# Kernel optimization log

Hardware: AMD Instinct MI355X
Metric: run time of the kernel (lower is better)

The kernel has to match this reference:

```python
import jax, jax.numpy as jnp
import numpy as np

H, I, B, S = 3200, 12800, 8, 1024  # InternViT-6B MLP dims


def setup_inputs() -> dict:
    key = jax.random.key(0)
    ks = jax.random.split(key, 8)
    # int8-valued activations/weights stored as int32 (harness dtype set)
    hidden_states = jax.random.randint(ks[0], (B, S, H), -127, 128, dtype=jnp.int32)
    scale = jax.random.uniform(ks[1], (B * S,), dtype=jnp.float32) * 1e-3 + 1e-5
    w1 = jax.random.randint(ks[2], (I, H), -127, 128, dtype=jnp.int32)
    w1_scale = jax.random.uniform(ks[3], (I,), dtype=jnp.float32) * 1e-3 + 1e-5
    b1 = jax.random.normal(ks[4], (I,), dtype=jnp.float32) * 0.02
    w2 = jax.random.randint(ks[5], (H, I), -127, 128, dtype=jnp.int32)
    w2_scale = jax.random.uniform(ks[6], (H,), dtype=jnp.float32) * 1e-3 + 1e-5
    b2 = jax.random.normal(ks[7], (H,), dtype=jnp.float32) * 0.02
    return {"hidden_states": hidden_states, "scale": scale, "w1": w1,
            "w1_scale": w1_scale, "b1": b1, "w2": w2, "w2_scale": w2_scale, "b2": b2}


def _w8a8_linear(x_q, x_scale, w_q, w_scale, b):
    # enough that fp32 matmul reproduces the exact integer accumulator to
    # within float32 rounding of the final sum.
    acc = jnp.matmul(x_q.astype(jnp.float32), w_q.astype(jnp.float32).T)  # [T, out]
    out = acc * x_scale[:, None] * w_scale[None, :] + b[None, :]
    return out.astype(jnp.float16)


def reference(hidden_states, scale, w1, w1_scale, b1, w2, w2_scale, b2):
    bsz, seq, hidden = hidden_states.shape
    x_q = hidden_states.reshape(-1, hidden)                 # [T, H] int8 values
    # fc1: W8A8 -> fp16 with dynamic per-token input scale
    fc1_out = _w8a8_linear(x_q, scale, w1, w1_scale, b1)    # [T, I] fp16
    # fused gelu_and_quant: exact GELU, then per-token dynamic int8 re-quant
    g = jax.nn.gelu(fc1_out.astype(jnp.float32), approximate=False)  # [T, I]
    new_scale = jnp.max(jnp.abs(g), axis=-1) / 127.0        # dynamic per-token scale
    act_q = jnp.clip(jnp.round(g / new_scale[:, None]), -127, 127)  # int8 values
    # fc2: W8A8 -> fp16
    out = _w8a8_linear(act_q, new_scale, w2, w2_scale, b2)  # [T, H] fp16
    return out
```

## Files before the change

kernel.cpp:

```cpp
#include <hip/hip_runtime.h>
#include <hip/hip_bf16.h>
#include <hip/hip_fp16.h>

#define T_DIM 8192
#define H_DIM 3200
#define I_DIM 12800

typedef int v4i __attribute__((ext_vector_type(4)));
typedef int v16i __attribute__((ext_vector_type(16)));
typedef _Float16 h8 __attribute__((ext_vector_type(8)));

__device__ __forceinline__ void gload16(const void* g, void* l) {
    __builtin_amdgcn_global_load_lds(
        (const __attribute__((address_space(1))) unsigned int*)g,
        (__attribute__((address_space(3))) unsigned int*)l, 16, 0, 0);
}

__global__ __launch_bounds__(256) void repack_kernel(const int* __restrict__ src,
                                                     unsigned int* __restrict__ dst,
                                                     long n4) {
    long i = (long)blockIdx.x * blockDim.x + threadIdx.x;
    long stride = (long)gridDim.x * blockDim.x;
    for (; i < n4; i += stride) {
        int4 v = ((const int4*)src)[i];
        dst[i] = (unsigned int)((v.x & 255) | ((v.y & 255) << 8) |
                                ((v.z & 255) << 16) | ((v.w & 255) << 24));
    }
}

template <int EPI>
__global__ __launch_bounds__(512, 2) void gemm_i8_32x32(
    const signed char* __restrict__ A, long strideA,
    const signed char* __restrict__ B, long strideB,
    int Ntrue, int K, int ldc,
    const float* __restrict__ rowscale, const float* __restrict__ colscale,
    const float* __restrict__ bias, void* __restrict__ Cout) {
    __shared__ signed char lds[131072];
    signed char* ldsA = lds;
    signed char* ldsB = lds + 65536;

    const int tid = threadIdx.x;
    const int lane = tid & 63, wid = tid >> 6;
    const int wr = wid >> 2, wc = wid & 3;
    const int bm = blockIdx.x, bn = blockIdx.y;
    const long Arow0 = (long)bm * 256;
    const long Bcol0 = (long)bn * 256;

    int g_row[2], g_cg[2];
#pragma unroll
    for (int u = 0; u < 2; ++u) {
        const int ch = tid + (u << 9);
        const int block = ch >> 7;
        const int p = ch & 127;
        const int half = (p >> 6) & 1;
        const int p6 = p & 63;
        const int r15 = p6 >> 2;
        const int col = p6 & 3;
        const int q = col ^ ((r15 >> 1) & 3);
        g_row[u] = block * 32 + ((q & 1) << 4) + r15;
        g_cg[u] = (half << 1) | (q >> 1);
    }
    const signed char* Ag0 = A + (Arow0 + g_row[0]) * strideA + g_cg[0] * 16;
    const signed char* Ag1 = A + (Arow0 + g_row[1]) * strideA + g_cg[1] * 16;
    const signed char* Bg0 = B + (Bcol0 + g_row[0]) * strideB + g_cg[0] * 16;
    const signed char* Bg1 = B + (Bcol0 + g_row[1]) * strideB + g_cg[1] * 16;
    const int d0 = tid * 16, d1 = (tid + 512) * 16;

    const int NH = K >> 6;

#define STAGE_A(h)                                  \
    {                                               \
        const int hc_ = (h) < NH ? (h) : NH - 1;    \
        const long ko_ = (long)hc_ << 6;            \
        signed char* d_ = ldsA + (((h) & 3) << 14); \
        gload16(Ag0 + ko_, d_ + d0);                \
        gload16(Ag1 + ko_, d_ + d1);                \
    }
#define STAGE_B(h)                                  \
    {                                               \
        const int hc_ = (h) < NH ? (h) : NH - 1;    \
        const long ko_ = (long)hc_ << 6;            \
        signed char* d_ = ldsB + (((h) & 3) << 14); \
        gload16(Bg0 + ko_, d_ + d0);                \
        gload16(Bg1 + ko_, d_ + d1);                \
    }

    const int rl = lane & 31, qh = lane >> 5;
    const int r15 = rl & 15, qb = rl >> 4;
    const int colr = ((qh << 1) | qb) ^ ((r15 >> 1) & 3);
    const int roff = r15 * 64 + colr * 16;
    const int aoff = (wr * 4) * 2048 + roff;
    const int boff = (wc * 2) * 2048 + roff;

    v16i acc[4][2] = {};

    STAGE_A(0); STAGE_B(0); STAGE_A(1); STAGE_B(1); STAGE_A(2); STAGE_B(2);
    asm volatile("s_waitcnt vmcnt(8)");
    __builtin_amdgcn_s_barrier();

    for (int h = 0; h < NH; ++h) {
        const signed char* sA = ldsA + ((h & 3) << 14);
        const signed char* sB = ldsB + ((h & 3) << 14);
        v4i a0[4], a1[4], b0[2], b1[2];
#pragma unroll
        for (int m = 0; m < 4; ++m) {
            a0[m] = *(const v4i*)(sA + aoff + m * 2048);
            a1[m] = *(const v4i*)(sA + aoff + m * 2048 + 1024);
        }
#pragma unroll
        for (int n = 0; n < 2; ++n) {
            b0[n] = *(const v4i*)(sB + boff + n * 2048);
            b1[n] = *(const v4i*)(sB + boff + n * 2048 + 1024);
        }
        STAGE_A(h + 3);
        STAGE_B(h + 3);
        __builtin_amdgcn_s_setprio(1);
#pragma unroll
        for (int m = 0; m < 4; ++m)
#pragma unroll
            for (int n = 0; n < 2; ++n)
                acc[m][n] = __builtin_amdgcn_mfma_i32_32x32x32_i8(
                    a0[m], b0[n], acc[m][n], 0, 0, 0);
#pragma unroll
        for (int m = 0; m < 4; ++m)
#pragma unroll
            for (int n = 0; n < 2; ++n)
                acc[m][n] = __builtin_amdgcn_mfma_i32_32x32x32_i8(
                    a1[m], b1[n], acc[m][n], 0, 0, 0);
        __builtin_amdgcn_s_setprio(0);
        asm volatile("s_waitcnt vmcnt(8)");
        __builtin_amdgcn_s_barrier();
    }

    const int row0 = bm * 256 + wr * 128;
    const int col0 = bn * 256 + wc * 64;
    const int rbase = 4 * qh;
#pragma unroll
    for (int m = 0; m < 4; ++m) {
#pragma unroll
        for (int n = 0; n < 2; ++n) {
            const int col = col0 + n * 32 + rl;
            if (col < Ntrue) {
                const float cs = colscale[col];
                const float bs = bias[col];
#pragma unroll
                for (int g = 0; g < 4; ++g) {
#pragma unroll
                    for (int rr = 0; rr < 4; ++rr) {
                        const int row = row0 + m * 32 + rbase + 8 * g + rr;
                        float v = (float)acc[m][n][g * 4 + rr];
                        v = __fmul_rn(v, rowscale[row]);
                        v = __fmul_rn(v, cs);
                        v = __fadd_rn(v, bs);
                        _Float16 hh = (_Float16)v;
                        const size_t idx = (size_t)row * ldc + col;
                        if (EPI == 0) ((_Float16*)Cout)[idx] = hh;
                        else ((float*)Cout)[idx] = (float)hh;
                    }
                }
            }
        }
    }
#undef STAGE_A
#undef STAGE_B
}

__global__ __launch_bounds__(256) void gelu_quant(_Float16* __restrict__ fc1,
                                                  float* __restrict__ nscale) {
    __shared__ float gbuf[I_DIM];
    __shared__ float wmax[4];
    const int tid = threadIdx.x, lane = tid & 63, wid = tid >> 6;
    const long t = blockIdx.x;
    const h8* row = (const h8*)(fc1 + t * I_DIM);
    float lmax = 0.f;
    for (int c = tid; c < I_DIM / 8; c += 256) {
        h8 v = row[c];
#pragma unroll
        for (int j = 0; j < 8; ++j) {
            float x = (float)v[j];
            float e = erff(__fdiv_rn(x, 1.41421356237309504880f));
            float g = __fmul_rn(__fmul_rn(0.5f, x), __fadd_rn(1.0f, e));
            gbuf[c * 8 + j] = g;
            lmax = fmaxf(lmax, fabsf(g));
        }
    }
#pragma unroll
    for (int off = 32; off; off >>= 1) lmax = fmaxf(lmax, __shfl_xor(lmax, off, 64));
    if (lane == 0) wmax[wid] = lmax;
    __syncthreads();
    const float gmax = fmaxf(fmaxf(wmax[0], wmax[1]), fmaxf(wmax[2], wmax[3]));
    const float ns = gmax / 127.0f;
    if (tid == 0) nscale[t] = ns;
    unsigned long long* out = (unsigned long long*)(fc1 + t * I_DIM);
    for (int c = tid; c < I_DIM / 8; c += 256) {
        unsigned long long pk = 0;
#pragma unroll
        for (int j = 0; j < 8; ++j) {
            float qv = rintf(__fdiv_rn(gbuf[c * 8 + j], ns));
            qv = fminf(fmaxf(qv, -127.f), 127.f);
            pk |= ((unsigned long long)(unsigned char)(signed char)(int)qv) << (8 * j);
        }
        out[c] = pk;
    }
}

extern "C" void kernel_launch(void* const* d_in, const int* in_sizes, int n_in,
                              void* d_out, int out_size, void* d_ws, size_t ws_size,
                              hipStream_t stream) {
    const int* hs = (const int*)d_in[0];
    const float* scale = (const float*)d_in[1];
    const int* w1 = (const int*)d_in[2];
    const float* w1s = (const float*)d_in[3];
    const float* b1 = (const float*)d_in[4];
    const int* w2 = (const int*)d_in[5];
    const float* w2s = (const float*)d_in[6];
    const float* b2 = (const float*)d_in[7];

    char* ws = (char*)d_ws;
    signed char* xq = (signed char*)ws;
    signed char* w1q = xq + (size_t)T_DIM * H_DIM;
    signed char* w2q = w1q + (size_t)I_DIM * H_DIM;
    _Float16* fc1h = (_Float16*)(w2q + (size_t)H_DIM * I_DIM);
    const size_t fixed = (size_t)T_DIM * H_DIM + 2 * (size_t)I_DIM * H_DIM;

    int nc = 1;
    while (nc < 16) {
        size_t need = fixed + ((size_t)T_DIM / nc) * I_DIM * 2 +
                      ((size_t)T_DIM / nc) * 4 + 256;
        if (need <= ws_size) break;
        nc <<= 1;
    }
    const int chunkT = T_DIM / nc;
    float* nscale = (float*)((char*)fc1h + (size_t)chunkT * I_DIM * 2);

    repack_kernel<<<2048, 256, 0, stream>>>(hs, (unsigned int*)xq, (long)T_DIM * H_DIM / 4);
    repack_kernel<<<2048, 256, 0, stream>>>(w1, (unsigned int*)w1q, (long)I_DIM * H_DIM / 4);
    repack_kernel<<<2048, 256, 0, stream>>>(w2, (unsigned int*)w2q, (long)H_DIM * I_DIM / 4);

    const int n2tiles = (H_DIM + 255) / 256;
    for (int c = 0; c < nc; ++c) {
        const int t0 = c * chunkT;
        gemm_i8_32x32<0><<<dim3(chunkT / 256, I_DIM / 256), 512, 0, stream>>>(
            xq + (size_t)t0 * H_DIM, (long)H_DIM, w1q, (long)H_DIM,
            I_DIM, H_DIM, I_DIM,
            scale + t0, w1s, b1, (void*)fc1h);
        gelu_quant<<<chunkT, 256, 0, stream>>>(fc1h, nscale);
        gemm_i8_32x32<1><<<dim3(chunkT / 256, n2tiles), 512, 0, stream>>>(
            (const signed char*)fc1h, (long)I_DIM * 2, w2q, (long)I_DIM,
            H_DIM, I_DIM, H_DIM,
            nscale, w2s, b2,
            (void*)((float*)d_out + (size_t)t0 * H_DIM));
    }
}
```

Before: 1.055 ms.

## Shrink int8 GEMM tiles to 128x128 with 256 threads and 3-stage LDS ring

Replaces the 256x256, 512-thread int8 MFMA GEMM with a 128x128 tile on 256 threads (four waves, each still 64x64). The LDS pipeline drops from four buffers to a three-slot rotating ring with a single combined A+B staging macro. LDS use falls from 128KB to 48KB and launch bounds target three blocks per CU. The goal is higher occupancy and a larger grid, and the fc2 N dimension (3200) now divides exactly by 128. In exchange, each tile does less data reuse per byte loaded, so global and L2 traffic goes up, and the prefetch distance is shorter.

```diff
diff --git a/kernel.cpp b/kernel.cpp
--- a/kernel.cpp
+++ b/kernel.cpp
@@ -29,27 +29,27 @@
 }
 
 template <int EPI>
-__global__ __launch_bounds__(512, 2) void gemm_i8_32x32(
+__global__ __launch_bounds__(256, 3) void gemm_i8_128(
     const signed char* __restrict__ A, long strideA,
     const signed char* __restrict__ B, long strideB,
     int Ntrue, int K, int ldc,
     const float* __restrict__ rowscale, const float* __restrict__ colscale,
     const float* __restrict__ bias, void* __restrict__ Cout) {
-    __shared__ signed char lds[131072];
+    __shared__ signed char lds[49152];
     signed char* ldsA = lds;
-    signed char* ldsB = lds + 65536;
+    signed char* ldsB = lds + 24576;
 
     const int tid = threadIdx.x;
     const int lane = tid & 63, wid = tid >> 6;
-    const int wr = wid >> 2, wc = wid & 3;
+    const int wr = wid >> 1, wc = wid & 1;
     const int bm = blockIdx.x, bn = blockIdx.y;
-    const long Arow0 = (long)bm * 256;
-    const long Bcol0 = (long)bn * 256;
+    const long Arow0 = (long)bm * 128;
+    const long Bcol0 = (long)bn * 128;
 
     int g_row[2], g_cg[2];
 #pragma unroll
     for (int u = 0; u < 2; ++u) {
-        const int ch = tid + (u << 9);
+        const int ch = tid + (u << 8);
         const int block = ch >> 7;
         const int p = ch & 127;
         const int half = (p >> 6) & 1;
@@ -64,46 +64,41 @@
     const signed char* Ag1 = A + (Arow0 + g_row[1]) * strideA + g_cg[1] * 16;
     const signed char* Bg0 = B + (Bcol0 + g_row[0]) * strideB + g_cg[0] * 16;
     const signed char* Bg1 = B + (Bcol0 + g_row[1]) * strideB + g_cg[1] * 16;
-    const int d0 = tid * 16, d1 = (tid + 512) * 16;
+    const int d0 = tid * 16, d1 = (tid + 256) * 16;
 
     const int NH = K >> 6;
 
-#define STAGE_A(h)                                  \
-    {                                               \
-        const int hc_ = (h) < NH ? (h) : NH - 1;    \
-        const long ko_ = (long)hc_ << 6;            \
-        signed char* d_ = ldsA + (((h) & 3) << 14); \
-        gload16(Ag0 + ko_, d_ + d0);                \
-        gload16(Ag1 + ko_, d_ + d1);                \
-    }
-#define STAGE_B(h)                                  \
-    {                                               \
-        const int hc_ = (h) < NH ? (h) : NH - 1;    \
-        const long ko_ = (long)hc_ << 6;            \
-        signed char* d_ = ldsB + (((h) & 3) << 14); \
-        gload16(Bg0 + ko_, d_ + d0);                \
-        gload16(Bg1 + ko_, d_ + d1);                \
+#define STAGE(h, so_)                            \
+    {                                            \
+        const int hc_ = (h) < NH ? (h) : NH - 1; \
+        const long ko_ = (long)hc_ << 6;         \
+        gload16(Ag0 + ko_, ldsA + (so_) + d0);   \
+        gload16(Ag1 + ko_, ldsA + (so_) + d1);   \
+        gload16(Bg0 + ko_, ldsB + (so_) + d0);   \
+        gload16(Bg1 + ko_, ldsB + (so_) + d1);   \
     }
 
     const int rl = lane & 31, qh = lane >> 5;
     const int r15 = rl & 15, qb = rl >> 4;
     const int colr = ((qh << 1) | qb) ^ ((r15 >> 1) & 3);
     const int roff = r15 * 64 + colr * 16;
-    const int aoff = (wr * 4) * 2048 + roff;
+    const int aoff = (wr * 2) * 2048 + roff;
     const int boff = (wc * 2) * 2048 + roff;
 
-    v16i acc[4][2] = {};
-
-    STAGE_A(0); STAGE_B(0); STAGE_A(1); STAGE_B(1); STAGE_A(2); STAGE_B(2);
-    asm volatile("s_waitcnt vmcnt(8)");
+    v16i acc[2][2] = {};
+
+    STAGE(0, 0);
+    STAGE(1, 8192);
+    asm volatile("s_waitcnt vmcnt(4)");
     __builtin_amdgcn_s_barrier();
 
+    int so_cur = 0, so_nxt = 8192, so_stg = 16384;
     for (int h = 0; h < NH; ++h) {
-        const signed char* sA = ldsA + ((h & 3) << 14);
-        const signed char* sB = ldsB + ((h & 3) << 14);
-        v4i a0[4], a1[4], b0[2], b1[2];
-#pragma unroll
-        for (int m = 0; m < 4; ++m) {
+        const signed char* sA = ldsA + so_cur;
+        const signed char* sB = ldsB + so_cur;
+        v4i a0[2], a1[2], b0[2], b1[2];
+#pragma unroll
+        for (int m = 0; m < 2; ++m) {
             a0[m] = *(const v4i*)(sA + aoff + m * 2048);
             a1[m] = *(const v4i*)(sA + aoff + m * 2048 + 1024);
         }
@@ -112,31 +107,34 @@
             b0[n] = *(const v4i*)(sB + boff + n * 2048);
             b1[n] = *(const v4i*)(sB + boff + n * 2048 + 1024);
         }
-        STAGE_A(h + 3);
-        STAGE_B(h + 3);
+        STAGE(h + 2, so_stg);
         __builtin_amdgcn_s_setprio(1);
 #pragma unroll
-        for (int m = 0; m < 4; ++m)
+        for (int m = 0; m < 2; ++m)
 #pragma unroll
             for (int n = 0; n < 2; ++n)
                 acc[m][n] = __builtin_amdgcn_mfma_i32_32x32x32_i8(
                     a0[m], b0[n], acc[m][n], 0, 0, 0);
 #pragma unroll
-        for (int m = 0; m < 4; ++m)
+        for (int m = 0; m < 2; ++m)
 #pragma unroll
             for (int n = 0; n < 2; ++n)
                 acc[m][n] = __builtin_amdgcn_mfma_i32_32x32x32_i8(
                     a1[m], b1[n], acc[m][n], 0, 0, 0);
         __builtin_amdgcn_s_setprio(0);
-        asm volatile("s_waitcnt vmcnt(8)");
+        asm volatile("s_waitcnt vmcnt(4)");
         __builtin_amdgcn_s_barrier();
-    }
-
-    const int row0 = bm * 256 + wr * 128;
-    const int col0 = bn * 256 + wc * 64;
+        const int t = so_cur;
+        so_cur = so_nxt;
+        so_nxt = so_stg;
+        so_stg = t;
+    }
+
+    const int row0 = bm * 128 + wr * 64;
+    const int col0 = bn * 128 + wc * 64;
     const int rbase = 4 * qh;
 #pragma unroll
-    for (int m = 0; m < 4; ++m) {
+    for (int m = 0; m < 2; ++m) {
 #pragma unroll
         for (int n = 0; n < 2; ++n) {
             const int col = col0 + n * 32 + rl;
@@ -161,8 +159,7 @@
             }
         }
     }
-#undef STAGE_A
-#undef STAGE_B
+#undef STAGE
 }
 
 __global__ __launch_bounds__(256) void gelu_quant(_Float16* __restrict__ fc1,
@@ -237,15 +234,14 @@
     repack_kernel<<<2048, 256, 0, stream>>>(w1, (unsigned int*)w1q, (long)I_DIM * H_DIM / 4);
     repack_kernel<<<2048, 256, 0, stream>>>(w2, (unsigned int*)w2q, (long)H_DIM * I_DIM / 4);
 
-    const int n2tiles = (H_DIM + 255) / 256;
     for (int c = 0; c < nc; ++c) {
         const int t0 = c * chunkT;
-        gemm_i8_32x32<0><<<dim3(chunkT / 256, I_DIM / 256), 512, 0, stream>>>(
+        gemm_i8_128<0><<<dim3(chunkT / 128, I_DIM / 128), 256, 0, stream>>>(
             xq + (size_t)t0 * H_DIM, (long)H_DIM, w1q, (long)H_DIM,
             I_DIM, H_DIM, I_DIM,
             scale + t0, w1s, b1, (void*)fc1h);
         gelu_quant<<<chunkT, 256, 0, stream>>>(fc1h, nscale);
-        gemm_i8_32x32<1><<<dim3(chunkT / 256, n2tiles), 512, 0, stream>>>(
+        gemm_i8_128<1><<<dim3(chunkT / 128, H_DIM / 128), 256, 0, stream>>>(
             (const signed char*)fc1h, (long)I_DIM * 2, w2q, (long)I_DIM,
             H_DIM, I_DIM, H_DIM,
             nscale, w2s, b2,
```

Result: slower. 1.278 ms (+21.1%).

## Double-buffer LDS fragments in registers to overlap reads with MFMAs

Applied to the files above, without the earlier changes.

The int8 GEMM main loop is unrolled by two and ping-pongs between two sets of register fragments. Each step loads the next k-step's A/B fragments from LDS before issuing the current step's MFMAs, so LDS read latency is hidden behind matrix math. The global-to-LDS wait is tightened from vmcnt(8) to vmcnt(4) so the stage read one step ahead has landed before the barrier. The cost is more VGPRs under a 512-thread, 2-block launch bound, which risks spills, and the unroll assumes an even number of k-steps.

```diff
diff --git a/kernel.cpp b/kernel.cpp
--- a/kernel.cpp
+++ b/kernel.cpp
@@ -29,7 +29,7 @@
 }
 
 template <int EPI>
-__global__ __launch_bounds__(512, 2) void gemm_i8_32x32(
+__global__ __launch_bounds__(512, 2) void gemm_i8_pf(
     const signed char* __restrict__ A, long strideA,
     const signed char* __restrict__ B, long strideB,
     int Ntrue, int K, int ldc,
@@ -95,41 +95,54 @@
     v16i acc[4][2] = {};
 
     STAGE_A(0); STAGE_B(0); STAGE_A(1); STAGE_B(1); STAGE_A(2); STAGE_B(2);
-    asm volatile("s_waitcnt vmcnt(8)");
+    asm volatile("s_waitcnt vmcnt(4)");
     __builtin_amdgcn_s_barrier();
 
-    for (int h = 0; h < NH; ++h) {
-        const signed char* sA = ldsA + ((h & 3) << 14);
-        const signed char* sB = ldsB + ((h & 3) << 14);
-        v4i a0[4], a1[4], b0[2], b1[2];
-#pragma unroll
-        for (int m = 0; m < 4; ++m) {
-            a0[m] = *(const v4i*)(sA + aoff + m * 2048);
-            a1[m] = *(const v4i*)(sA + aoff + m * 2048 + 1024);
-        }
-#pragma unroll
-        for (int n = 0; n < 2; ++n) {
-            b0[n] = *(const v4i*)(sB + boff + n * 2048);
-            b1[n] = *(const v4i*)(sB + boff + n * 2048 + 1024);
-        }
-        STAGE_A(h + 3);
-        STAGE_B(h + 3);
-        __builtin_amdgcn_s_setprio(1);
-#pragma unroll
-        for (int m = 0; m < 4; ++m)
-#pragma unroll
-            for (int n = 0; n < 2; ++n)
-                acc[m][n] = __builtin_amdgcn_mfma_i32_32x32x32_i8(
-                    a0[m], b0[n], acc[m][n], 0, 0, 0);
-#pragma unroll
-        for (int m = 0; m < 4; ++m)
-#pragma unroll
-            for (int n = 0; n < 2; ++n)
-                acc[m][n] = __builtin_amdgcn_mfma_i32_32x32x32_i8(
-                    a1[m], b1[n], acc[m][n], 0, 0, 0);
-        __builtin_amdgcn_s_setprio(0);
-        asm volatile("s_waitcnt vmcnt(8)");
-        __builtin_amdgcn_s_barrier();
+    v4i a0c[4], a1c[4], b0c[2], b1c[2];
+    v4i a0n[4], a1n[4], b0n[2], b1n[2];
+#pragma unroll
+    for (int m = 0; m < 4; ++m) {
+        a0c[m] = *(const v4i*)(ldsA + aoff + m * 2048);
+        a1c[m] = *(const v4i*)(ldsA + aoff + m * 2048 + 1024);
+    }
+#pragma unroll
+    for (int n = 0; n < 2; ++n) {
+        b0c[n] = *(const v4i*)(ldsB + boff + n * 2048);
+        b1c[n] = *(const v4i*)(ldsB + boff + n * 2048 + 1024);
+    }
+
+#define PHASE(h, A0C, A1C, B0C, B1C, A0N, A1N, B0N, B1N)                  \
+    {                                                                     \
+        const int hn_ = ((h) + 1 < NH) ? (h) + 1 : NH - 1;                \
+        const signed char* sA_ = ldsA + ((hn_ & 3) << 14);                \
+        const signed char* sB_ = ldsB + ((hn_ & 3) << 14);                \
+        _Pragma("unroll") for (int m = 0; m < 4; ++m) {                   \
+            A0N[m] = *(const v4i*)(sA_ + aoff + m * 2048);                \
+            A1N[m] = *(const v4i*)(sA_ + aoff + m * 2048 + 1024);         \
+        }                                                                 \
+        _Pragma("unroll") for (int n = 0; n < 2; ++n) {                   \
+            B0N[n] = *(const v4i*)(sB_ + boff + n * 2048);                \
+            B1N[n] = *(const v4i*)(sB_ + boff + n * 2048 + 1024);         \
+        }                                                                 \
+        STAGE_A((h) + 3);                                                 \
+        STAGE_B((h) + 3);                                                 \
+        __builtin_amdgcn_s_setprio(1);                                    \
+        _Pragma("unroll") for (int m = 0; m < 4; ++m)                     \
+            _Pragma("unroll") for (int n = 0; n < 2; ++n)                 \
+                acc[m][n] = __builtin_amdgcn_mfma_i32_32x32x32_i8(        \
+                    A0C[m], B0C[n], acc[m][n], 0, 0, 0);                  \
+        _Pragma("unroll") for (int m = 0; m < 4; ++m)                     \
+            _Pragma("unroll") for (int n = 0; n < 2; ++n)                 \
+                acc[m][n] = __builtin_amdgcn_mfma_i32_32x32x32_i8(        \
+                    A1C[m], B1C[n], acc[m][n], 0, 0, 0);                  \
+        __builtin_amdgcn_s_setprio(0);                                    \
+        asm volatile("s_waitcnt vmcnt(4)");                               \
+        __builtin_amdgcn_s_barrier();                                     \
+    }
+
+    for (int h = 0; h < NH; h += 2) {
+        PHASE(h, a0c, a1c, b0c, b1c, a0n, a1n, b0n, b1n);
+        PHASE(h + 1, a0n, a1n, b0n, b1n, a0c, a1c, b0c, b1c);
     }
 
     const int row0 = bm * 256 + wr * 128;
@@ -161,6 +174,7 @@
             }
         }
     }
+#undef PHASE
 #undef STAGE_A
 #undef STAGE_B
 }
@@ -240,12 +254,12 @@
     const int n2tiles = (H_DIM + 255) / 256;
     for (int c = 0; c < nc; ++c) {
         const int t0 = c * chunkT;
-        gemm_i8_32x32<0><<<dim3(chunkT / 256, I_DIM / 256), 512, 0, stream>>>(
+        gemm_i8_pf<0><<<dim3(chunkT / 256, I_DIM / 256), 512, 0, stream>>>(
             xq + (size_t)t0 * H_DIM, (long)H_DIM, w1q, (long)H_DIM,
             I_DIM, H_DIM, I_DIM,
             scale + t0, w1s, b1, (void*)fc1h);
         gelu_quant<<<chunkT, 256, 0, stream>>>(fc1h, nscale);
-        gemm_i8_32x32<1><<<dim3(chunkT / 256, n2tiles), 512, 0, stream>>>(
+        gemm_i8_pf<1><<<dim3(chunkT / 256, n2tiles), 512, 0, stream>>>(
             (const signed char*)fc1h, (long)I_DIM * 2, w2q, (long)I_DIM,
             H_DIM, I_DIM, H_DIM,
             nscale, w2s, b2,
```

Result: no change. 1.046 ms (-0.9%).
